# Optimization experiments

Measured on AMD Instinct MI355X. Metric: run time of the kernel, lower is better.

The kernel has to match this reference:

```python
import jax, jax.numpy as jnp
import numpy as np

WS = 7   # window size
SS = 3   # shift size
NH = 8   # num heads
DIM = 256
HH = 56
WW = 56
B = 32


def _layernorm(z, g, b):
    m = z.mean(-1, keepdims=True)
    v = ((z - m) ** 2).mean(-1, keepdims=True)
    return (z - m) / jnp.sqrt(v + 1e-6) * g + b


def _win_partition(z, ws):
    Bd, H, W, C = z.shape
    z = z.reshape(Bd, H // ws, ws, W // ws, ws, C).transpose(0, 1, 3, 2, 4, 5)
    return z.reshape(-1, ws * ws, C)


def _win_reverse(w, ws, Bd, H, W, C):
    w = w.reshape(Bd, H // ws, W // ws, ws, ws, C).transpose(0, 1, 3, 2, 4, 5)
    return w.reshape(Bd, H, W, C)


def _forward(x, attn_mask, rel_pos_index, H, W,
             norm1_g, norm1_b, qkv_w, qkv_b, temperature, rel_table,
             proj_w, proj_b, norm2_g, norm2_b, fc1_w, fc1_b, fc2_w, fc2_b):
    Bd, L, C = x.shape
    hd = C // NH
    N = WS * WS
    shortcut = x
    z = _layernorm(x, norm1_g, norm1_b).reshape(Bd, H, W, C)
    # cyclic shift (H,W divisible by WS -> no padding branch)
    z = jnp.roll(z, (-SS, -SS), axis=(1, 2))
    zw = _win_partition(z, WS)                      # (B*nW, N, C)
    qkv = (zw @ qkv_w + qkv_b).reshape(-1, N, 3, NH, hd).transpose(2, 0, 3, 1, 4)
    q, k, v = qkv[0], qkv[1], qkv[2]                # (B*nW, NH, N, hd)
    attn = jnp.einsum('bhnd,bhmd->bhnm', q, k) * jnp.exp(temperature)
    # LSA diagonal mask (applied BEFORE bias/shift-mask, as in the TF code)
    neg = jnp.finfo(attn.dtype).min
    attn = jnp.where(jnp.eye(N, dtype=bool), neg, attn)
    bias = rel_table[rel_pos_index.reshape(-1)].reshape(N, N, NH).transpose(2, 0, 1)
    attn = attn + bias[None]
    nW = attn_mask.shape[0]
    attn = attn.reshape(Bd, nW, NH, N, N) + attn_mask[None, :, None]
    attn = jax.nn.softmax(attn.reshape(-1, NH, N, N), axis=-1)
    o = jnp.einsum('bhnm,bhmd->bhnd', attn, v).transpose(0, 2, 1, 3).reshape(-1, N, C)
    o = o @ proj_w + proj_b
    o = _win_reverse(o, WS, Bd, H, W, C)
    o = jnp.roll(o, (SS, SS), axis=(1, 2)).reshape(Bd, H * W, C)
    x = shortcut + o
    h = _layernorm(x, norm2_g, norm2_b)
    h = jax.nn.gelu(h @ fc1_w + fc1_b, approximate=False) @ fc2_w + fc2_b
    return x + h


def setup_inputs() -> dict:
    key = jax.random.key(0)
    ks = jax.random.split(key, 8)
    C = DIM
    hd = C // NH
    tn = lambda k, s: jax.random.normal(k, s, jnp.float32) * 0.02
    x = jax.random.normal(ks[0], (B, HH * WW, C), jnp.float32)
    # relative position index (numpy, identical to the TF build())
    coords = np.stack(np.meshgrid(np.arange(WS), np.arange(WS), indexing='ij')).reshape(2, -1)
    rel = (coords[:, :, None] - coords[:, None, :]).transpose(1, 2, 0).astype(np.int64)
    rel[:, :, 0] += WS - 1
    rel[:, :, 1] += WS - 1
    rel[:, :, 0] *= 2 * WS - 1
    rel_pos_index = jnp.asarray(rel.sum(-1), jnp.int32)   # (49,49)
    # shifted-window attention mask (standard Swin construction)
    img_mask = np.zeros((1, HH, WW, 1), np.float32)
    cnt = 0
    for hs in (slice(0, -WS), slice(-WS, -SS), slice(-SS, None)):
        for ws_ in (slice(0, -WS), slice(-WS, -SS), slice(-SS, None)):
            img_mask[:, hs, ws_, :] = cnt
            cnt += 1
    mw = img_mask.reshape(1, HH // WS, WS, WW // WS, WS, 1).transpose(0, 1, 3, 2, 4, 5).reshape(-1, WS * WS)
    am = mw[:, None, :] - mw[:, :, None]
    attn_mask = jnp.asarray(np.where(am != 0, -100.0, 0.0).astype(np.float32))  # (64,49,49)
    return {
        'x': x,
        'attn_mask': attn_mask,
        'norm1_g': jnp.ones((C,), jnp.float32),
        'norm1_b': jnp.zeros((C,), jnp.float32),
        'qkv_w': tn(ks[1], (C, 3 * C)),
        'qkv_b': jnp.zeros((3 * C,), jnp.float32),
        'temperature': jnp.asarray(np.log(hd ** (-0.5)), jnp.float32),
        'rel_table': tn(ks[2], ((2 * WS - 1) ** 2, NH)),
        'proj_w': tn(ks[3], (C, C)),
        'proj_b': jnp.zeros((C,), jnp.float32),
        'norm2_g': jnp.ones((C,), jnp.float32),
        'norm2_b': jnp.zeros((C,), jnp.float32),
        'fc1_w': tn(ks[4], (C, 4 * C)),
        'fc1_b': jnp.zeros((4 * C,), jnp.float32),
        'fc2_w': tn(ks[5], (4 * C, C)),
        'fc2_b': jnp.zeros((C,), jnp.float32),
        'rel_pos_index': rel_pos_index,
        'H': HH,
        'W': WW,
    }


def reference(x, attn_mask, norm1_g, norm1_b, qkv_w, qkv_b, temperature, rel_table,
              proj_w, proj_b, norm2_g, norm2_b, fc1_w, fc1_b, fc2_w, fc2_b,
              rel_pos_index, H, W):
    return _forward(x, attn_mask, rel_pos_index, H, W,
                    norm1_g, norm1_b, qkv_w, qkv_b, temperature, rel_table,
                    proj_w, proj_b, norm2_g, norm2_b, fc1_w, fc1_b, fc2_w, fc2_b)
```

## Files before the change

kernel.cpp:

```cpp
#include <hip/hip_runtime.h>

typedef unsigned short u16;
typedef unsigned int u32;
typedef _Float16 h4 __attribute__((ext_vector_type(4)));
typedef _Float16 h8 __attribute__((ext_vector_type(8)));
typedef float f32x4 __attribute__((ext_vector_type(4)));

#define MFMA16(a, b, c) __builtin_amdgcn_mfma_f32_16x16x32_f16((a), (b), (c), 0, 0, 0)

__device__ __forceinline__ float wsum(float v) {
  #pragma unroll
  for (int o = 32; o > 0; o >>= 1) v += __shfl_down(v, o);
  return __shfl(v, 0);
}

__global__ void k_prep_qkv(const float* __restrict__ w, _Float16* __restrict__ o) {
  const int e = blockIdx.x * 256 + threadIdx.x;
  const int r = e >> 8, k = e & 255;
  const int h = r / 96, rem = r - h * 96;
  const int mat = rem >> 5, cc = rem & 31;
  o[e] = (_Float16)w[k * 768 + mat * 256 + h * 32 + cc];
}

__global__ void k_prep_pw(const float* __restrict__ w, _Float16* __restrict__ o) {
  const int e = blockIdx.x * 256 + threadIdx.x;
  const int oc = e >> 8, ic = e & 255;
  o[e] = (_Float16)w[ic * 256 + oc];
}

__global__ void k_prep_w1(const float* __restrict__ w, _Float16* __restrict__ o) {
  const int e = blockIdx.x * 256 + threadIdx.x;
  const int col = e >> 8, k = e & 255;
  o[e] = (_Float16)w[k * 1024 + col];
}

__global__ void k_prep_w2(const float* __restrict__ w, _Float16* __restrict__ o) {
  const int e = blockIdx.x * 256 + threadIdx.x;
  const int oc = e >> 10, k = e & 1023;
  o[e] = (_Float16)w[k * 256 + oc];
}

__global__ void k_prep_btab(const int* __restrict__ rpi, const float* __restrict__ rtab,
                            float* __restrict__ btab) {
  const int e = blockIdx.x * 256 + threadIdx.x;
  if (e < 2401) {
    const int idx = rpi[e];
    #pragma unroll
    for (int h = 0; h < 8; ++h) btab[h * 2401 + e] = rtab[idx * 8 + h];
  }
}

__global__ __launch_bounds__(512, 2) void k_attn(
    const float* __restrict__ x, const _Float16* __restrict__ wsq,
    const _Float16* __restrict__ pwh, const float* __restrict__ qkvb,
    const float* __restrict__ g1, const float* __restrict__ b1,
    const float* __restrict__ temp, const float* __restrict__ btab,
    const float* __restrict__ amask, const float* __restrict__ pb,
    float* __restrict__ io) {
  __shared__ __align__(16) char smem[131072];
  const int tid = threadIdx.x;
  const int lane = tid & 63, w = tid >> 6;
  const int lr = lane & 15, lk = lane >> 4;
  const int win = blockIdx.x;
  const int bb = win >> 6, wimg = win & 63;
  const int hb = wimg >> 3, wb = wimg & 7;
  const float scale = expf(temp[0]);
  char* const pwv = smem + 32768 + w * 12288;

  {
    const float4 gz = ((const float4*)g1)[lane];
    const float4 bz = ((const float4*)b1)[lane];
    for (int n = w; n < 49; n += 8) {
      int i = n / 7, j = n - 7 * i;
      int rs = hb * 7 + i + 3; if (rs >= 56) rs -= 56;
      int cs = wb * 7 + j + 3; if (cs >= 56) cs -= 56;
      const float4 p = ((const float4*)(x + ((size_t)bb * 3136 + rs * 56 + cs) * 256))[lane];
      float mean = wsum(p.x + p.y + p.z + p.w) * (1.f / 256.f);
      float d0 = p.x - mean, d1 = p.y - mean, d2 = p.z - mean, d3 = p.w - mean;
      float var = wsum(d0 * d0 + d1 * d1 + d2 * d2 + d3 * d3) * (1.f / 256.f);
      float rstd = rsqrtf(var + 1e-6f);
      h4 z;
      z[0] = (_Float16)(d0 * rstd * gz.x + bz.x);
      z[1] = (_Float16)(d1 * rstd * gz.y + bz.y);
      z[2] = (_Float16)(d2 * rstd * gz.z + bz.z);
      z[3] = (_Float16)(d3 * rstd * gz.w + bz.w);
      *(h4*)(smem + ((n * 512 + lane * 8) ^ ((n & 7) << 4))) = z;
    }
  }
  __syncthreads();

  {
    f32x4 zz = {0.f, 0.f, 0.f, 0.f};
    f32x4 acc[4][6];
    #pragma unroll
    for (int t = 0; t < 4; ++t)
      #pragma unroll
      for (int c = 0; c < 6; ++c) acc[t][c] = zz;
    const _Float16* wr[6];
    #pragma unroll
    for (int c = 0; c < 6; ++c)
      wr[c] = wsq + ((size_t)(w * 96 + c * 16 + lr) * 256 + lk * 8);
    const int swzA = (lr & 7) << 4;
    #pragma unroll
    for (int ks = 0; ks < 8; ++ks) {
      const int ko = ks * 64 + lk * 16;
      h8 a[4];
      #pragma unroll
      for (int t = 0; t < 4; ++t)
        a[t] = *(const h8*)(smem + (((t * 16 + lr) * 512 + ko) ^ swzA));
      h8 b[6];
      #pragma unroll
      for (int c = 0; c < 6; ++c) b[c] = *(const h8*)(wr[c] + ks * 32);
      #pragma unroll
      for (int t = 0; t < 4; ++t)
        #pragma unroll
        for (int c = 0; c < 6; ++c) acc[t][c] = MFMA16(a[t], b[c], acc[t][c]);
    }
    #pragma unroll
    for (int c = 0; c < 6; ++c) {
      const int mat = c >> 1;
      const int cc = (c & 1) * 16 + lr;
      const float bias = qkvb[mat * 256 + w * 32 + cc];
      #pragma unroll
      for (int t = 0; t < 4; ++t) {
        const int tok0 = t * 16 + lk * 4;
        if (mat == 2) {
          h4 pk;
          #pragma unroll
          for (int r = 0; r < 4; ++r) {
            float v = (tok0 + r < 49) ? (acc[t][c][r] + bias) : 0.f;
            pk[r] = (_Float16)v;
          }
          *(h4*)(pwv + 8192 + (tok0 >> 3) * 512 + cc * 16 + (tok0 & 7) * 2) = pk;
        } else {
          char* base = pwv + (mat ? 4096 : 0);
          const float mult = mat ? 1.f : scale;
          #pragma unroll
          for (int r = 0; r < 4; ++r) {
            const int tok = tok0 + r;
            float v = (tok < 49) ? (acc[t][c][r] + bias) * mult : 0.f;
            *(_Float16*)(base + ((tok * 64 + cc * 2) ^ (((tok >> 1) & 3) << 4))) = (_Float16)v;
          }
        }
      }
    }
  }
  __syncthreads();

  {
    f32x4 zz = {0.f, 0.f, 0.f, 0.f};
    f32x4 s[4][4];
    #pragma unroll
    for (int t = 0; t < 4; ++t)
      #pragma unroll
      for (int m = 0; m < 4; ++m) s[t][m] = zz;
    const int swzq = ((lr >> 1) & 3) << 4;
    h8 aq[4], bk[4];
    #pragma unroll
    for (int t = 0; t < 4; ++t) {
      aq[t] = *(const h8*)(pwv + (((t * 16 + lr) * 64 + lk * 16) ^ swzq));
      bk[t] = *(const h8*)(pwv + 4096 + (((t * 16 + lr) * 64 + lk * 16) ^ swzq));
    }
    #pragma unroll
    for (int t = 0; t < 4; ++t)
      #pragma unroll
      for (int m = 0; m < 4; ++m) s[t][m] = MFMA16(aq[t], bk[m], s[t][m]);

    const float* bt = btab + (size_t)w * 2401;
    const float* am = amask + (size_t)wimg * 2401;
    #pragma unroll
    for (int t = 0; t < 4; ++t) {
      #pragma unroll
      for (int r = 0; r < 4; ++r) {
        const int n = t * 16 + lk * 4 + r;
        if (n < 49) {
          #pragma unroll
          for (int m = 0; m < 4; ++m) {
            const int mm = m * 16 + lr;
            float sv;
            if (mm >= 49) sv = -1e38f;
            else {
              sv = s[t][m][r];
              if (mm == n) sv = -1e30f;
              const int ee = n * 49 + mm;
              sv += bt[ee] + am[ee];
            }
            s[t][m][r] = sv;
          }
        } else {
          #pragma unroll
          for (int m = 0; m < 4; ++m) s[t][m][r] = 0.f;
        }
      }
    }
    #pragma unroll
    for (int t = 0; t < 4; ++t) {
      #pragma unroll
      for (int r = 0; r < 4; ++r) {
        float mx = fmaxf(fmaxf(s[t][0][r], s[t][1][r]), fmaxf(s[t][2][r], s[t][3][r]));
        mx = fmaxf(mx, __shfl_xor(mx, 1));
        mx = fmaxf(mx, __shfl_xor(mx, 2));
        mx = fmaxf(mx, __shfl_xor(mx, 4));
        mx = fmaxf(mx, __shfl_xor(mx, 8));
        float e0 = expf(s[t][0][r] - mx), e1 = expf(s[t][1][r] - mx);
        float e2 = expf(s[t][2][r] - mx), e3 = expf(s[t][3][r] - mx);
        float sm = e0 + e1 + e2 + e3;
        sm += __shfl_xor(sm, 1);
        sm += __shfl_xor(sm, 2);
        sm += __shfl_xor(sm, 4);
        sm += __shfl_xor(sm, 8);
        const float inv = 1.f / sm;
        const int n = t * 16 + lk * 4 + r;
        const int sw = (n & 7) << 4;
        char* pr = pwv + n * 128;
        *(_Float16*)(pr + ((lr * 2) ^ sw))          = (_Float16)(e0 * inv);
        *(_Float16*)(pr + (((16 + lr) * 2) ^ sw))   = (_Float16)(e1 * inv);
        *(_Float16*)(pr + (((32 + lr) * 2) ^ sw))   = (_Float16)(e2 * inv);
        *(_Float16*)(pr + (((48 + lr) * 2) ^ sw))   = (_Float16)(e3 * inv);
      }
    }
  }

  {
    f32x4 zz = {0.f, 0.f, 0.f, 0.f};
    f32x4 o0[4], o1[4];
    #pragma unroll
    for (int t = 0; t < 4; ++t) { o0[t] = zz; o1[t] = zz; }
    const int swzp = (lr & 7) << 4;
    #pragma unroll
    for (int ks = 0; ks < 2; ++ks) {
      h8 bv0 = *(const h8*)(pwv + 8192 + (ks * 4 + lk) * 512 + lr * 16);
      h8 bv1 = *(const h8*)(pwv + 8192 + (ks * 4 + lk) * 512 + (16 + lr) * 16);
      #pragma unroll
      for (int t = 0; t < 4; ++t) {
        h8 ap = *(const h8*)(pwv + (((t * 16 + lr) * 128 + ks * 64 + lk * 16) ^ swzp));
        o0[t] = MFMA16(ap, bv0, o0[t]);
        o1[t] = MFMA16(ap, bv1, o1[t]);
      }
    }
    #pragma unroll
    for (int t = 0; t < 4; ++t) {
      #pragma unroll
      for (int r = 0; r < 4; ++r) {
        const int tok = t * 16 + lk * 4 + r;
        const int sw = (tok & 7) << 4;
        char* orow = smem + tok * 512;
        *(_Float16*)(orow + (((w * 32 + lr) * 2) ^ sw))      = (_Float16)o0[t][r];
        *(_Float16*)(orow + (((w * 32 + 16 + lr) * 2) ^ sw)) = (_Float16)o1[t][r];
      }
    }
  }
  __syncthreads();

  {
    f32x4 zz = {0.f, 0.f, 0.f, 0.f};
    f32x4 oacc[4][2];
    #pragma unroll
    for (int t = 0; t < 4; ++t) { oacc[t][0] = zz; oacc[t][1] = zz; }
    const int swzA = (lr & 7) << 4;
    const _Float16* pwr = pwh + (size_t)(w * 32 + lr) * 256 + lk * 8;
    #pragma unroll
    for (int ks = 0; ks < 8; ++ks) {
      const int ko = ks * 64 + lk * 16;
      h8 b0 = *(const h8*)(pwr + ks * 32);
      h8 b1 = *(const h8*)(pwr + 16 * 256 + ks * 32);
      #pragma unroll
      for (int t = 0; t < 4; ++t) {
        h8 a = *(const h8*)(smem + (((t * 16 + lr) * 512 + ko) ^ swzA));
        oacc[t][0] = MFMA16(a, b0, oacc[t][0]);
        oacc[t][1] = MFMA16(a, b1, oacc[t][1]);
      }
    }
    const float pb0 = pb[w * 32 + lr];
    const float pb1 = pb[w * 32 + 16 + lr];
    #pragma unroll
    for (int t = 0; t < 4; ++t) {
      #pragma unroll
      for (int r = 0; r < 4; ++r) {
        const int tok = t * 16 + lk * 4 + r;
        if (tok < 49) {
          const int i = tok / 7, j = tok - 7 * i;
          int rs = hb * 7 + i + 3; if (rs >= 56) rs -= 56;
          int cs = wb * 7 + j + 3; if (cs >= 56) cs -= 56;
          const size_t ro = ((size_t)bb * 3136 + rs * 56 + cs) * 256 + w * 32 + lr;
          io[ro]      = x[ro]      + oacc[t][0][r] + pb0;
          io[ro + 16] = x[ro + 16] + oacc[t][1][r] + pb1;
        }
      }
    }
  }
}

#define MH_OFF 32768

__global__ __launch_bounds__(512, 4) void k_mlp2(
    float* __restrict__ io, const float* __restrict__ g2, const float* __restrict__ b2,
    const _Float16* __restrict__ w1h, const float* __restrict__ fb1,
    const _Float16* __restrict__ w2h, const float* __restrict__ fb2) {
  __shared__ __align__(16) char smem[65536];
  const int tid = threadIdx.x;
  const int lane = tid & 63, w = tid >> 6;
  const int lr = lane & 15, lk = lane >> 4;
  const size_t t0 = (size_t)blockIdx.x * 64;
  const int swz = (lr & 7) << 4;

  {
    const float4 gz = ((const float4*)g2)[lane];
    const float4 bz = ((const float4*)b2)[lane];
    for (int n = w; n < 64; n += 8) {
      const float4 p = ((const float4*)(io + (t0 + n) * 256))[lane];
      float mean = wsum(p.x + p.y + p.z + p.w) * (1.f / 256.f);
      float d0 = p.x - mean, d1 = p.y - mean, d2 = p.z - mean, d3 = p.w - mean;
      float var = wsum(d0 * d0 + d1 * d1 + d2 * d2 + d3 * d3) * (1.f / 256.f);
      float rstd = rsqrtf(var + 1e-6f);
      h4 z;
      z[0] = (_Float16)(d0 * rstd * gz.x + bz.x);
      z[1] = (_Float16)(d1 * rstd * gz.y + bz.y);
      z[2] = (_Float16)(d2 * rstd * gz.z + bz.z);
      z[3] = (_Float16)(d3 * rstd * gz.w + bz.w);
      *(h4*)(smem + ((n * 512 + lane * 8) ^ ((n & 7) << 4))) = z;
    }
  }
  __syncthreads();

  f32x4 zz = {0.f, 0.f, 0.f, 0.f};
  f32x4 oacc[4][2];
  #pragma unroll
  for (int t = 0; t < 4; ++t) { oacc[t][0] = zz; oacc[t][1] = zz; }

  for (int ch = 0; ch < 4; ++ch) {
    f32x4 facc[4][2];
    #pragma unroll
    for (int t = 0; t < 4; ++t) { facc[t][0] = zz; facc[t][1] = zz; }
    {
      const _Float16* w1p = w1h + (size_t)(ch * 256 + w * 32 + lr) * 256 + lk * 8;
      #pragma unroll
      for (int ks = 0; ks < 8; ++ks) {
        const int ko = ks * 64 + lk * 16;
        h8 b0 = *(const h8*)(w1p + ks * 32);
        h8 b1 = *(const h8*)(w1p + 16 * 256 + ks * 32);
        #pragma unroll
        for (int t = 0; t < 4; ++t) {
          h8 a = *(const h8*)(smem + (((t * 16 + lr) * 512 + ko) ^ swz));
          facc[t][0] = MFMA16(a, b0, facc[t][0]);
          facc[t][1] = MFMA16(a, b1, facc[t][1]);
        }
      }
    }
    #pragma unroll
    for (int nt = 0; nt < 2; ++nt) {
      const float bb = fb1[ch * 256 + w * 32 + nt * 16 + lr];
      #pragma unroll
      for (int t = 0; t < 4; ++t) {
        #pragma unroll
        for (int r = 0; r < 4; ++r) {
          float a = facc[t][nt][r] + bb;
          float gl = 0.5f * a * (1.f + erff(a * 0.70710678118654752f));
          const int tok = t * 16 + lk * 4 + r;
          *(_Float16*)(smem + MH_OFF +
                       ((tok * 512 + w * 64 + nt * 32 + lr * 2) ^ ((tok & 7) << 4))) =
              (_Float16)gl;
        }
      }
    }
    __syncthreads();
    {
      const _Float16* w2p = w2h + (size_t)(w * 32 + lr) * 1024 + ch * 256 + lk * 8;
      #pragma unroll
      for (int ks = 0; ks < 8; ++ks) {
        const int ko = ks * 64 + lk * 16;
        h8 b0 = *(const h8*)(w2p + ks * 32);
        h8 b1 = *(const h8*)(w2p + 16 * 1024 + ks * 32);
        #pragma unroll
        for (int t = 0; t < 4; ++t) {
          h8 a = *(const h8*)(smem + MH_OFF + (((t * 16 + lr) * 512 + ko) ^ swz));
          oacc[t][0] = MFMA16(a, b0, oacc[t][0]);
          oacc[t][1] = MFMA16(a, b1, oacc[t][1]);
        }
      }
    }
    __syncthreads();
  }

  #pragma unroll
  for (int nt = 0; nt < 2; ++nt) {
    const float bv = fb2[w * 32 + nt * 16 + lr];
    #pragma unroll
    for (int t = 0; t < 4; ++t) {
      #pragma unroll
      for (int r = 0; r < 4; ++r) {
        const int tok = t * 16 + lk * 4 + r;
        const size_t idx = (t0 + tok) * 256 + (size_t)(w * 32 + nt * 16 + lr);
        io[idx] = io[idx] + oacc[t][nt][r] + bv;
      }
    }
  }
}

extern "C" void kernel_launch(void* const* d_in, const int* in_sizes, int n_in,
                              void* d_out, int out_size, void* d_ws, size_t ws_size,
                              hipStream_t stream) {
  const float* x     = (const float*)d_in[0];
  const float* amask = (const float*)d_in[1];
  const float* g1    = (const float*)d_in[2];
  const float* b1    = (const float*)d_in[3];
  const float* qkvw  = (const float*)d_in[4];
  const float* qkvb  = (const float*)d_in[5];
  const float* temp  = (const float*)d_in[6];
  const float* rtab  = (const float*)d_in[7];
  const float* pw    = (const float*)d_in[8];
  const float* pb    = (const float*)d_in[9];
  const float* g2    = (const float*)d_in[10];
  const float* b2    = (const float*)d_in[11];
  const float* w1    = (const float*)d_in[12];
  const float* fb1   = (const float*)d_in[13];
  const float* w2    = (const float*)d_in[14];
  const float* fb2   = (const float*)d_in[15];
  const int* rpi     = (const int*)d_in[16];

  char* ws = (char*)d_ws;
  _Float16* wsq = (_Float16*)ws;
  _Float16* pwh = (_Float16*)(ws + 393216);
  _Float16* w1h = (_Float16*)(ws + 524288);
  _Float16* w2h = (_Float16*)(ws + 1048576);
  float* btab   = (float*)(ws + 1572864);
  float* io = (float*)d_out;

  k_prep_qkv<<<768, 256, 0, stream>>>(qkvw, wsq);
  k_prep_pw<<<256, 256, 0, stream>>>(pw, pwh);
  k_prep_w1<<<1024, 256, 0, stream>>>(w1, w1h);
  k_prep_w2<<<1024, 256, 0, stream>>>(w2, w2h);
  k_prep_btab<<<10, 256, 0, stream>>>(rpi, rtab, btab);
  k_attn<<<2048, 512, 0, stream>>>(x, wsq, pwh, qkvb, g1, b1, temp, btab,
                                   amask, pb, io);
  k_mlp2<<<1568, 512, 0, stream>>>(io, g2, b2, w1h, fb1, w2h, fb2);
}
```

Before: 851.5 us.

## Fuse MLP block into attention kernel, keeping residual tile in shared memory

Merges the separate MLP kernel into the per-window attention kernel. The post-attention residual for each window's 49 tokens is held in swizzled shared memory, then LayerNorm2, FC1+GELU and FC2 run on it before a single write to global memory. This removes a global write/read round trip of the intermediate activations and one kernel launch. The MLP now runs on 64-row tiles with only 49 valid rows (padding rows are zero), so some MFMA work is wasted, and occupancy is set by the larger 128KB shared-memory attention kernel rather than the MLP's earlier 4-blocks setting.

After: 843.1 us. No clear change (-1.0%).

```diff
diff --git a/kernel.cpp b/kernel.cpp
--- a/kernel.cpp
+++ b/kernel.cpp
@@ -7,6 +7,7 @@
 typedef float f32x4 __attribute__((ext_vector_type(4)));
 
 #define MFMA16(a, b, c) __builtin_amdgcn_mfma_f32_16x16x32_f16((a), (b), (c), 0, 0, 0)
+#define SW(t) ((((t) >> 2) & 3) << 5)
 
 __device__ __forceinline__ float wsum(float v) {
   #pragma unroll
@@ -50,12 +51,18 @@
   }
 }
 
-__global__ __launch_bounds__(512, 2) void k_attn(
+#define X1_OFF 65536
+#define MH_OFF 32768
+
+__global__ __launch_bounds__(512, 2) void k_blk(
     const float* __restrict__ x, const _Float16* __restrict__ wsq,
     const _Float16* __restrict__ pwh, const float* __restrict__ qkvb,
     const float* __restrict__ g1, const float* __restrict__ b1,
     const float* __restrict__ temp, const float* __restrict__ btab,
     const float* __restrict__ amask, const float* __restrict__ pb,
+    const float* __restrict__ g2, const float* __restrict__ b2,
+    const _Float16* __restrict__ w1h, const float* __restrict__ fb1,
+    const _Float16* __restrict__ w2h, const float* __restrict__ fb2,
     float* __restrict__ io) {
   __shared__ __align__(16) char smem[131072];
   const int tid = threadIdx.x;
@@ -278,37 +285,28 @@
       #pragma unroll
       for (int r = 0; r < 4; ++r) {
         const int tok = t * 16 + lk * 4 + r;
+        float v0 = 0.f, v1 = 0.f;
         if (tok < 49) {
           const int i = tok / 7, j = tok - 7 * i;
           int rs = hb * 7 + i + 3; if (rs >= 56) rs -= 56;
           int cs = wb * 7 + j + 3; if (cs >= 56) cs -= 56;
           const size_t ro = ((size_t)bb * 3136 + rs * 56 + cs) * 256 + w * 32 + lr;
-          io[ro]      = x[ro]      + oacc[t][0][r] + pb0;
-          io[ro + 16] = x[ro + 16] + oacc[t][1][r] + pb1;
-        }
-      }
-    }
-  }
-}
-
-#define MH_OFF 32768
-
-__global__ __launch_bounds__(512, 4) void k_mlp2(
-    float* __restrict__ io, const float* __restrict__ g2, const float* __restrict__ b2,
-    const _Float16* __restrict__ w1h, const float* __restrict__ fb1,
-    const _Float16* __restrict__ w2h, const float* __restrict__ fb2) {
-  __shared__ __align__(16) char smem[65536];
-  const int tid = threadIdx.x;
-  const int lane = tid & 63, w = tid >> 6;
-  const int lr = lane & 15, lk = lane >> 4;
-  const size_t t0 = (size_t)blockIdx.x * 64;
-  const int swz = (lr & 7) << 4;
+          v0 = x[ro]      + oacc[t][0][r] + pb0;
+          v1 = x[ro + 16] + oacc[t][1][r] + pb1;
+        }
+        char* xr = smem + X1_OFF + tok * 1024;
+        *(float*)(xr + (((w * 32 + lr) * 4)      ^ SW(tok))) = v0;
+        *(float*)(xr + (((w * 32 + 16 + lr) * 4) ^ SW(tok))) = v1;
+      }
+    }
+  }
+  __syncthreads();
 
   {
     const float4 gz = ((const float4*)g2)[lane];
     const float4 bz = ((const float4*)b2)[lane];
     for (int n = w; n < 64; n += 8) {
-      const float4 p = ((const float4*)(io + (t0 + n) * 256))[lane];
+      const float4 p = *(const float4*)(smem + X1_OFF + n * 1024 + ((lane * 16) ^ SW(n)));
       float mean = wsum(p.x + p.y + p.z + p.w) * (1.f / 256.f);
       float d0 = p.x - mean, d1 = p.y - mean, d2 = p.z - mean, d3 = p.w - mean;
       float var = wsum(d0 * d0 + d1 * d1 + d2 * d2 + d3 * d3) * (1.f / 256.f);
@@ -323,15 +321,16 @@
   }
   __syncthreads();
 
-  f32x4 zz = {0.f, 0.f, 0.f, 0.f};
-  f32x4 oacc[4][2];
+  f32x4 zzm = {0.f, 0.f, 0.f, 0.f};
+  f32x4 macc[4][2];
   #pragma unroll
-  for (int t = 0; t < 4; ++t) { oacc[t][0] = zz; oacc[t][1] = zz; }
+  for (int t = 0; t < 4; ++t) { macc[t][0] = zzm; macc[t][1] = zzm; }
+  const int swz = (lr & 7) << 4;
 
   for (int ch = 0; ch < 4; ++ch) {
     f32x4 facc[4][2];
     #pragma unroll
-    for (int t = 0; t < 4; ++t) { facc[t][0] = zz; facc[t][1] = zz; }
+    for (int t = 0; t < 4; ++t) { facc[t][0] = zzm; facc[t][1] = zzm; }
     {
       const _Float16* w1p = w1h + (size_t)(ch * 256 + w * 32 + lr) * 256 + lk * 8;
       #pragma unroll
@@ -349,12 +348,12 @@
     }
     #pragma unroll
     for (int nt = 0; nt < 2; ++nt) {
-      const float bb = fb1[ch * 256 + w * 32 + nt * 16 + lr];
+      const float bb2 = fb1[ch * 256 + w * 32 + nt * 16 + lr];
       #pragma unroll
       for (int t = 0; t < 4; ++t) {
         #pragma unroll
         for (int r = 0; r < 4; ++r) {
-          float a = facc[t][nt][r] + bb;
+          float a = facc[t][nt][r] + bb2;
           float gl = 0.5f * a * (1.f + erff(a * 0.70710678118654752f));
           const int tok = t * 16 + lk * 4 + r;
           *(_Float16*)(smem + MH_OFF +
@@ -374,26 +373,38 @@
         #pragma unroll
         for (int t = 0; t < 4; ++t) {
           h8 a = *(const h8*)(smem + MH_OFF + (((t * 16 + lr) * 512 + ko) ^ swz));
-          oacc[t][0] = MFMA16(a, b0, oacc[t][0]);
-          oacc[t][1] = MFMA16(a, b1, oacc[t][1]);
+          macc[t][0] = MFMA16(a, b0, macc[t][0]);
+          macc[t][1] = MFMA16(a, b1, macc[t][1]);
         }
       }
     }
     __syncthreads();
   }
 
-  #pragma unroll
-  for (int nt = 0; nt < 2; ++nt) {
-    const float bv = fb2[w * 32 + nt * 16 + lr];
+  {
+    const float bv0 = fb2[w * 32 + lr];
+    const float bv1 = fb2[w * 32 + 16 + lr];
     #pragma unroll
     for (int t = 0; t < 4; ++t) {
       #pragma unroll
       for (int r = 0; r < 4; ++r) {
         const int tok = t * 16 + lk * 4 + r;
-        const size_t idx = (t0 + tok) * 256 + (size_t)(w * 32 + nt * 16 + lr);
-        io[idx] = io[idx] + oacc[t][nt][r] + bv;
-      }
-    }
+        char* xr = smem + X1_OFF + tok * 1024;
+        float* p0 = (float*)(xr + (((w * 32 + lr) * 4)      ^ SW(tok)));
+        float* p1 = (float*)(xr + (((w * 32 + 16 + lr) * 4) ^ SW(tok)));
+        *p0 += macc[t][0][r] + bv0;
+        *p1 += macc[t][1][r] + bv1;
+      }
+    }
+  }
+  __syncthreads();
+
+  for (int n = w; n < 49; n += 8) {
+    const int i = n / 7, j = n - 7 * i;
+    int rs = hb * 7 + i + 3; if (rs >= 56) rs -= 56;
+    int cs = wb * 7 + j + 3; if (cs >= 56) cs -= 56;
+    const float4 v = *(const float4*)(smem + X1_OFF + n * 1024 + ((lane * 16) ^ SW(n)));
+    *(float4*)(io + ((size_t)bb * 3136 + rs * 56 + cs) * 256 + lane * 4) = v;
   }
 }
 
@@ -431,7 +442,6 @@
   k_prep_w1<<<1024, 256, 0, stream>>>(w1, w1h);
   k_prep_w2<<<1024, 256, 0, stream>>>(w2, w2h);
   k_prep_btab<<<10, 256, 0, stream>>>(rpi, rtab, btab);
-  k_attn<<<2048, 512, 0, stream>>>(x, wsq, pwh, qkvb, g1, b1, temp, btab,
-                                   amask, pb, io);
-  k_mlp2<<<1568, 512, 0, stream>>>(io, g2, b2, w1h, fb1, w2h, fb2);
-}
+  k_blk<<<2048, 512, 0, stream>>>(x, wsq, pwh, qkvb, g1, b1, temp, btab,
+                                  amask, pb, g2, b2, w1h, fb1, w2h, fb2, io);
+}
```
